# Optimization experiments

Hardware: AMD Instinct MI355X
Metric: run time of the kernel (lower is better)

The kernel has to match this reference:

```python
import jax, jax.numpy as jnp
import numpy as np

DIM = 512
HEADS = 8
HEAD_DIM = DIM // HEADS
SR = 2
LN_EPS = 1e-3  # keras LayerNormalization default epsilon


def setup_inputs() -> dict:
    key = jax.random.key(0)
    ks = jax.random.split(key, 12)
    B, N = 4, 64 * 64
    s = lambda fan_in: 1.0 / np.sqrt(fan_in)
    return {
        "x": jax.random.normal(ks[0], (B, N, DIM), dtype=jnp.float32),
        "H": 64,
        "W": 64,
        "Wq": jax.random.normal(ks[1], (DIM, DIM), jnp.float32) * s(DIM),
        "bq": jnp.zeros((DIM,), jnp.float32),
        "Wkv": jax.random.normal(ks[2], (DIM, 2 * DIM), jnp.float32) * s(DIM),
        "bkv": jnp.zeros((2 * DIM,), jnp.float32),
        "Wp": jax.random.normal(ks[3], (DIM, DIM), jnp.float32) * s(DIM),
        "bp": jnp.zeros((DIM,), jnp.float32),
        "sr_kernel": jax.random.normal(ks[4], (SR, SR, DIM, DIM), jnp.float32) * s(SR * SR * DIM),
        "sr_bias": jnp.zeros((DIM,), jnp.float32),
        "gamma": jnp.ones((DIM,), jnp.float32),
        "beta": jnp.zeros((DIM,), jnp.float32),
    }


def _layer_norm(x, gamma, beta):
    mu = jnp.mean(x, axis=-1, keepdims=True)
    var = jnp.mean(jnp.square(x - mu), axis=-1, keepdims=True)
    return (x - mu) * jax.lax.rsqrt(var + LN_EPS) * gamma + beta


def reference(x, H, W, Wq, bq, Wkv, bkv, Wp, bp, sr_kernel, sr_bias, gamma, beta):
    B, N, C = x.shape
    scale = HEAD_DIM ** -0.5

    # q projection -> [B, heads, N, head_dim]
    q = (x @ Wq + bq).reshape(B, N, HEADS, HEAD_DIM).transpose(0, 2, 1, 3)

    # sequence reduction: strided conv (kernel=stride=SR, SAME padding) + LayerNorm
    x_ = x.reshape(B, H, W, C)
    x_ = jax.lax.conv_general_dilated(
        x_, sr_kernel, window_strides=(SR, SR), padding="SAME",
        dimension_numbers=("NHWC", "HWIO", "NHWC")) + sr_bias
    x_ = x_.reshape(B, -1, C)           # [B, N_kv, C]
    x_ = _layer_norm(x_, gamma, beta)

    # kv projection -> k, v: [B, heads, N_kv, head_dim]
    kv = (x_ @ Wkv + bkv).reshape(B, -1, 2, HEADS, HEAD_DIM).transpose(2, 0, 3, 1, 4)
    k, v = kv[0], kv[1]

    attn = jnp.einsum("bhnd,bhmd->bhnm", q, k) * scale
    attn = jax.nn.softmax(attn, axis=-1)
    out = jnp.einsum("bhnm,bhmd->bhnd", attn, v)  # [B, heads, N, head_dim]
    out = out.transpose(0, 2, 1, 3).reshape(B, N, C)
    return out @ Wp + bp
```

## Files before the change

### kernel.cpp

```cpp
#include <hip/hip_runtime.h>
#include <math.h>

#define BDIM   4
#define NTOK   4096
#define CDIM   512
#define NHEADS 8
#define HDIM   64
#define NKV    1024
#define HPIX   64
#define WPIX   64

typedef __attribute__((ext_vector_type(8)))  short    short8;
typedef __attribute__((ext_vector_type(4)))  float    floatx4;
typedef __attribute__((ext_vector_type(16))) float    floatx16;
typedef __attribute__((ext_vector_type(4)))  unsigned uintx4;
typedef unsigned short ushort_t;

static __device__ inline unsigned short f2bf(float f) {
  unsigned u = __float_as_uint(f);
  unsigned r = (u + 0x7fffu + ((u >> 16) & 1u)) >> 16;
  return (unsigned short)r;
}

static __device__ inline unsigned cvt_pk_bf16(float lo, float hi) {
  unsigned r;
  asm volatile("v_cvt_pk_bf16_f32 %0, %1, %2" : "=v"(r) : "v"(lo), "v"(hi));
  return r;
}

static __device__ inline void pl32_swap(unsigned& a, unsigned& b) {
  asm volatile("v_permlane32_swap_b32 %0, %1" : "+v"(a), "+v"(b));
}

static __device__ inline void gload16(const void* g, void* l) {
  __builtin_amdgcn_global_load_lds(
      (const __attribute__((address_space(1))) void*)g,
      (__attribute__((address_space(3))) void*)l, 16, 0, 0);
}

__global__ __launch_bounds__(256) void prep_kernel(
    const float* __restrict__ x, ushort_t* __restrict__ xb,
    const float* __restrict__ Wq, const float* __restrict__ Wkv,
    const float* __restrict__ Wp, const float* __restrict__ srk,
    ushort_t* __restrict__ Wqt, ushort_t* __restrict__ Wkvt,
    ushort_t* __restrict__ Wpt, ushort_t* __restrict__ srkt) {
  const int bid = blockIdx.x;
  if (bid < 4096) {
    const size_t i = ((size_t)bid * 256 + threadIdx.x) * 8;
    float4 f0 = *(const float4*)&x[i];
    float4 f1 = *(const float4*)&x[i + 4];
    short8 v;
    v[0] = (short)f2bf(f0.x); v[1] = (short)f2bf(f0.y);
    v[2] = (short)f2bf(f0.z); v[3] = (short)f2bf(f0.w);
    v[4] = (short)f2bf(f1.x); v[5] = (short)f2bf(f1.y);
    v[6] = (short)f2bf(f1.z); v[7] = (short)f2bf(f1.w);
    *(short8*)&xb[i] = v;
    return;
  }
  __shared__ float t[32][33];
  const int tb = bid - 4096;
  const float* in; ushort_t* outp; int C, tile;
  if (tb < 256)       { in = Wq;  outp = Wqt;  C = 512;  tile = tb; }
  else if (tb < 768)  { in = Wkv; outp = Wkvt; C = 1024; tile = tb - 256; }
  else if (tb < 1024) { in = Wp;  outp = Wpt;  C = 512;  tile = tb - 768; }
  else                { in = srk; outp = srkt; C = 512;  tile = tb - 1024; }
  const int R = (tb >= 1024) ? 2048 : 512;
  const int tcn = C >> 5;
  const int r0 = (tile / tcn) * 32, c0 = (tile % tcn) * 32;
  const int tr = threadIdx.x & 31, tc = threadIdx.x >> 5;
#pragma unroll
  for (int i = 0; i < 4; ++i)
    t[tc + 8 * i][tr] = in[(size_t)(r0 + tc + 8 * i) * C + c0 + tr];
  __syncthreads();
#pragma unroll
  for (int i = 0; i < 4; ++i)
    outp[(size_t)(c0 + tc + 8 * i) * R + r0 + tr] = f2bf(t[tr][tc + 8 * i]);
}

__global__ __launch_bounds__(256) void gemm_bf16(
    const ushort_t* __restrict__ A, const ushort_t* __restrict__ Bt,
    const float* __restrict__ bias, float* __restrict__ Cf,
    ushort_t* __restrict__ Cb, int M, int N, int K, float scale) {
  __shared__ char As[16384];
  __shared__ char Bs[16384];
  const int tid = threadIdx.x;
  const int w = tid >> 6, lane = tid & 63;
  const int g = lane >> 4, qr = lane & 15;
  const int wr = w >> 1, wc = w & 1;
  const int row0 = blockIdx.x * 128, col0 = blockIdx.y * 128;
  const int rl = w * 8 + (lane >> 3);
  const int sch = (lane & 7) ^ ((lane >> 3) & 7);

  floatx4 acc[4][4] = {};

  for (int k0 = 0; k0 < K; k0 += 64) {
    __syncthreads();
#pragma unroll
    for (int i = 0; i < 4; ++i) {
      const int r = rl + 32 * i;
      const unsigned lb = (unsigned)(w * 1024 + i * 4096);
      gload16(&A[(size_t)(row0 + r) * K + k0 + sch * 8], As + lb);
      gload16(&Bt[(size_t)(col0 + r) * K + k0 + sch * 8], Bs + lb);
    }
    __syncthreads();

#pragma unroll
    for (int kc = 0; kc < 2; ++kc) {
      short8 af[4], bfr[4];
#pragma unroll
      for (int mi = 0; mi < 4; ++mi) {
        const int r = wr * 64 + mi * 16 + qr;
        af[mi] = *(const short8*)(As +
            ((unsigned)(r * 128 + kc * 64 + g * 16) ^ (unsigned)((r & 7) << 4)));
      }
#pragma unroll
      for (int ni = 0; ni < 4; ++ni) {
        const int c = wc * 64 + ni * 16 + qr;
        bfr[ni] = *(const short8*)(Bs +
            ((unsigned)(c * 128 + kc * 64 + g * 16) ^ (unsigned)((c & 7) << 4)));
      }
#pragma unroll
      for (int mi = 0; mi < 4; ++mi)
#pragma unroll
        for (int ni = 0; ni < 4; ++ni)
          acc[mi][ni] = __builtin_amdgcn_mfma_f32_16x16x32_bf16(
              af[mi], bfr[ni], acc[mi][ni], 0, 0, 0);
    }
  }

#pragma unroll
  for (int mi = 0; mi < 4; ++mi) {
#pragma unroll
    for (int ni = 0; ni < 4; ++ni) {
      const int col = col0 + wc * 64 + ni * 16 + qr;
      const float bv = bias[col];
#pragma unroll
      for (int ri = 0; ri < 4; ++ri) {
        const int row = row0 + wr * 64 + mi * 16 + g * 4 + ri;
        const float v = (acc[mi][ni][ri] + bv) * scale;
        if (Cb) Cb[(size_t)row * N + col] = f2bf(v);
        else    Cf[(size_t)row * N + col] = v;
      }
    }
  }
}

__global__ __launch_bounds__(256) void gemm_kv(
    const ushort_t* __restrict__ A, const ushort_t* __restrict__ Bt,
    const float* __restrict__ bias, char* __restrict__ Kimg,
    char* __restrict__ Vimg) {
  __shared__ char As[16384];
  __shared__ char Bs[16384];
  const int tid = threadIdx.x;
  const int w = tid >> 6, lane = tid & 63;
  const int g = lane >> 4, qr = lane & 15;
  const int wr = w >> 1, wc = w & 1;
  const int row0 = blockIdx.x * 128, col0 = blockIdx.y * 128;
  const int rl = w * 8 + (lane >> 3);
  const int sch = (lane & 7) ^ ((lane >> 3) & 7);

  floatx4 acc[4][4] = {};

  for (int k0 = 0; k0 < 512; k0 += 64) {
    __syncthreads();
#pragma unroll
    for (int i = 0; i < 4; ++i) {
      const int r = rl + 32 * i;
      const unsigned lb = (unsigned)(w * 1024 + i * 4096);
      gload16(&A[(size_t)(row0 + r) * 512 + k0 + sch * 8], As + lb);
      gload16(&Bt[(size_t)(col0 + r) * 512 + k0 + sch * 8], Bs + lb);
    }
    __syncthreads();

#pragma unroll
    for (int kc = 0; kc < 2; ++kc) {
      short8 af[4], bfr[4];
#pragma unroll
      for (int mi = 0; mi < 4; ++mi) {
        const int r = wr * 64 + mi * 16 + qr;
        af[mi] = *(const short8*)(As +
            ((unsigned)(r * 128 + kc * 64 + g * 16) ^ (unsigned)((r & 7) << 4)));
      }
#pragma unroll
      for (int ni = 0; ni < 4; ++ni) {
        const int c = wc * 64 + ni * 16 + qr;
        bfr[ni] = *(const short8*)(Bs +
            ((unsigned)(c * 128 + kc * 64 + g * 16) ^ (unsigned)((c & 7) << 4)));
      }
#pragma unroll
      for (int mi = 0; mi < 4; ++mi)
#pragma unroll
        for (int ni = 0; ni < 4; ++ni)
          acc[mi][ni] = __builtin_amdgcn_mfma_f32_16x16x32_bf16(
              af[mi], bfr[ni], acc[mi][ni], 0, 0, 0);
    }
  }

#pragma unroll
  for (int mi = 0; mi < 4; ++mi) {
#pragma unroll
    for (int ni = 0; ni < 4; ++ni) {
      const int col = col0 + wc * 64 + ni * 16 + qr;
      const float bv = bias[col];
#pragma unroll
      for (int ri = 0; ri < 4; ++ri) {
        const int row = row0 + wr * 64 + mi * 16 + g * 4 + ri;
        const ushort_t v = f2bf(acc[mi][ni][ri] + bv);
        const int b = row >> 10, m = row & 1023;
        const int t = m >> 6, mr = m & 63;
        const int st = mr >> 5;
        if (col < 512) {
          const int h = col >> 6, d = col & 63;
          const int ql = mr & 31;
          const int ks = d >> 4, hi2 = (d >> 3) & 1, j = d & 7;
          char* img = Kimg + (((size_t)(b * NHEADS + h) * 16 + t) << 13);
          *(ushort_t*)(img + (unsigned)(((st * 4 + ks) << 10) +
                       ((hi2 << 5) + ql) * 16 + j * 2)) = v;
        } else {
          const int c = col - 512, h = c >> 6, d = c & 63;
          const int r5 = mr & 31;
          const int hf16 = r5 >> 4, rem = r5 & 15;
          const int hi2 = rem >> 3, cc = (rem >> 1) & 3, odd = rem & 1;
          const int db = d >> 5, ql = d & 31;
          char* img = Vimg + (((size_t)(b * NHEADS + h) * 16 + t) << 13);
          *(ushort_t*)(img + (unsigned)(((st * 4 + db * 2 + hf16) << 10) +
                       ((hi2 << 5) + ql) * 16 + cc * 4 + odd * 2)) = v;
        }
      }
    }
  }
}

__global__ __launch_bounds__(256) void conv_gemm(
    const ushort_t* __restrict__ xb, const ushort_t* __restrict__ Bt,
    const float* __restrict__ bias, float* __restrict__ Cf) {
  __shared__ char As[16384];
  __shared__ char Bs[8192];
  const int tid = threadIdx.x;
  const int w = tid >> 6, lane = tid & 63;
  const int g = lane >> 4, qr = lane & 15;
  const int wr = w >> 1, wc = w & 1;
  const int row0 = blockIdx.x * 128, col0 = blockIdx.y * 64;
  const int rl = w * 8 + (lane >> 3);
  const int sch = (lane & 7) ^ ((lane >> 3) & 7);

  floatx4 acc[4][2] = {};

  for (int k0 = 0; k0 < 2048; k0 += 64) {
    __syncthreads();
    {
      const int di = k0 >> 10, dj = (k0 >> 9) & 1, cib = (k0 & 511) + sch * 8;
#pragma unroll
      for (int i = 0; i < 4; ++i) {
        const int r = rl + 32 * i;
        const int gr = row0 + r;
        const int bb = gr >> 10, p = gr & 1023;
        const int oi = p >> 5, oj = p & 31;
        const size_t off =
            ((size_t)((bb * HPIX + 2 * oi + di) * WPIX + 2 * oj + dj)) * CDIM + cib;
        gload16(&xb[off], As + (unsigned)(w * 1024 + i * 4096));
      }
#pragma unroll
      for (int i = 0; i < 2; ++i) {
        const int r = rl + 32 * i;
        gload16(&Bt[(size_t)(col0 + r) * 2048 + k0 + sch * 8],
                Bs + (unsigned)(w * 1024 + i * 4096));
      }
    }
    __syncthreads();

#pragma unroll
    for (int kc = 0; kc < 2; ++kc) {
      short8 af[4], bfr[2];
#pragma unroll
      for (int mi = 0; mi < 4; ++mi) {
        const int r = wr * 64 + mi * 16 + qr;
        af[mi] = *(const short8*)(As +
            ((unsigned)(r * 128 + kc * 64 + g * 16) ^ (unsigned)((r & 7) << 4)));
      }
#pragma unroll
      for (int ni = 0; ni < 2; ++ni) {
        const int c = wc * 32 + ni * 16 + qr;
        bfr[ni] = *(const short8*)(Bs +
            ((unsigned)(c * 128 + kc * 64 + g * 16) ^ (unsigned)((c & 7) << 4)));
      }
#pragma unroll
      for (int mi = 0; mi < 4; ++mi)
#pragma unroll
        for (int ni = 0; ni < 2; ++ni)
          acc[mi][ni] = __builtin_amdgcn_mfma_f32_16x16x32_bf16(
              af[mi], bfr[ni], acc[mi][ni], 0, 0, 0);
    }
  }

#pragma unroll
  for (int mi = 0; mi < 4; ++mi) {
#pragma unroll
    for (int ni = 0; ni < 2; ++ni) {
      const int col = col0 + wc * 32 + ni * 16 + qr;
      const float bv = bias[col];
#pragma unroll
      for (int ri = 0; ri < 4; ++ri) {
        const int row = row0 + wr * 64 + mi * 16 + g * 4 + ri;
        Cf[(size_t)row * 512 + col] = acc[mi][ni][ri] + bv;
      }
    }
  }
}

__global__ __launch_bounds__(256) void ln_kernel(
    const float* __restrict__ in, ushort_t* __restrict__ out,
    const float* __restrict__ gamma, const float* __restrict__ beta) {
  const int row = blockIdx.x * 4 + (threadIdx.x >> 6);
  const int lane = threadIdx.x & 63;
  const float* p = in + (size_t)row * CDIM;
  float v[8];
  float s = 0.f;
#pragma unroll
  for (int j = 0; j < 8; ++j) { v[j] = p[lane + j * 64]; s += v[j]; }
#pragma unroll
  for (int o = 32; o > 0; o >>= 1) s += __shfl_xor(s, o);
  const float mu = s * (1.0f / 512.0f);
  float vs = 0.f;
#pragma unroll
  for (int j = 0; j < 8; ++j) { const float d = v[j] - mu; vs += d * d; }
#pragma unroll
  for (int o = 32; o > 0; o >>= 1) vs += __shfl_xor(vs, o);
  const float rstd = rsqrtf(vs * (1.0f / 512.0f) + 1e-3f);
  ushort_t* q = out + (size_t)row * CDIM;
#pragma unroll
  for (int j = 0; j < 8; ++j) {
    const int c = lane + j * 64;
    q[c] = f2bf((v[j] - mu) * rstd * gamma[c] + beta[c]);
  }
}

__global__ __launch_bounds__(256) void attn_kernel(
    const ushort_t* __restrict__ Q, const char* __restrict__ Kimg,
    const char* __restrict__ Vimg, ushort_t* __restrict__ AO) {
  __shared__ char Ks[16384];
  __shared__ char Vt[16384];
  __shared__ float red[4][32];

  const int b = blockIdx.z, h = blockIdx.y;
  const int q0 = blockIdx.x * 128;
  const int tid = threadIdx.x;
  const int w = tid >> 6, lane = tid & 63;
  const int ql = lane & 31;
  const int hi = lane >> 5;
  const unsigned lbyte = (unsigned)(lane * 16);

  short8 qf[4];
  {
    const ushort_t* qp = &Q[((size_t)(b * NTOK + q0 + 32 * w + ql)) * CDIM + h * HDIM];
#pragma unroll
    for (int ks = 0; ks < 4; ++ks)
      qf[ks] = *(const short8*)&qp[ks * 16 + hi * 8];
  }

  const char* kbase = Kimg + (((size_t)(b * NHEADS + h)) << 17);
  const char* vbase = Vimg + (((size_t)(b * NHEADS + h)) << 17);

  floatx16 Oacc[2] = {};
  float l0 = 0.f, l1 = 0.f;

  for (int t2 = 0; t2 < NKV / 128; ++t2) {
    __syncthreads();
    {
      const char* kg = kbase + ((size_t)t2 << 14) + w * 4096 + lane * 16;
      const char* vg = vbase + ((size_t)t2 << 14) + w * 4096 + lane * 16;
      char* kd = Ks + w * 4096;
      char* vd = Vt + w * 4096;
#pragma unroll
      for (int i = 0; i < 4; ++i) {
        gload16(kg + i * 1024, kd + i * 1024);
        gload16(vg + i * 1024, vd + i * 1024);
      }
    }
    __syncthreads();

#pragma unroll
    for (int sub = 0; sub < 2; ++sub) {
      const char* ksb = Ks + sub * 8192 + lbyte;
      const char* vtb = Vt + sub * 8192 + lbyte;

      floatx16 sacc[2];
      __builtin_amdgcn_s_setprio(1);
#pragma unroll
      for (int st = 0; st < 2; ++st) {
        floatx16 s_ = {};
#pragma unroll
        for (int ks = 0; ks < 4; ++ks) {
          short8 kf = *(const short8*)(ksb + ((st * 4 + ks) << 10));
          s_ = __builtin_amdgcn_mfma_f32_32x32x16_bf16(kf, qf[ks], s_, 0, 0, 0);
        }
        sacc[st] = s_;
      }
      __builtin_amdgcn_s_setprio(0);

#pragma unroll
      for (int st = 0; st < 2; ++st) {
        unsigned W[8];
#pragma unroll
        for (int i = 0; i < 8; ++i) {
          const float pa = __builtin_amdgcn_exp2f(sacc[st][2 * i]);
          const float pb = __builtin_amdgcn_exp2f(sacc[st][2 * i + 1]);
          l0 += pa; l1 += pb;
          W[i] = cvt_pk_bf16(pa, pb);
        }
        pl32_swap(W[0], W[2]); pl32_swap(W[1], W[3]);
        pl32_swap(W[4], W[6]); pl32_swap(W[5], W[7]);
        uintx4 u0 = {W[0], W[1], W[2], W[3]};
        uintx4 u1 = {W[4], W[5], W[6], W[7]};
        const short8 pa0 = __builtin_bit_cast(short8, u0);
        const short8 pa1 = __builtin_bit_cast(short8, u1);
        __builtin_amdgcn_s_setprio(1);
#pragma unroll
        for (int db = 0; db < 2; ++db) {
          short8 v0 = *(const short8*)(vtb + ((st * 4 + db * 2) << 10));
          short8 v1 = *(const short8*)(vtb + ((st * 4 + db * 2 + 1) << 10));
          Oacc[db] = __builtin_amdgcn_mfma_f32_32x32x16_bf16(pa0, v0, Oacc[db], 0, 0, 0);
          Oacc[db] = __builtin_amdgcn_mfma_f32_32x32x16_bf16(pa1, v1, Oacc[db], 0, 0, 0);
        }
        __builtin_amdgcn_s_setprio(0);
      }
    }
  }

  float lrun = l0 + l1;
  lrun += __shfl_xor(lrun, 32);
  if (hi == 0) red[w][ql] = 1.0f / lrun;
  asm volatile("s_waitcnt lgkmcnt(0)" ::: "memory");
  __builtin_amdgcn_sched_barrier(0);
#pragma unroll
  for (int r = 0; r < 16; ++r) {
    const int qrow = (r & 3) + 8 * (r >> 2) + 4 * hi;
    const float iv = red[w][qrow];
    const size_t rowoff =
        ((size_t)(b * NTOK + q0 + 32 * w + qrow)) * CDIM + h * HDIM;
    AO[rowoff + ql]      = f2bf(Oacc[0][r] * iv);
    AO[rowoff + 32 + ql] = f2bf(Oacc[1][r] * iv);
  }
}

extern "C" void kernel_launch(void* const* d_in, const int* in_sizes, int n_in,
                              void* d_out, int out_size, void* d_ws, size_t ws_size,
                              hipStream_t stream) {
  const float* x     = (const float*)d_in[0];
  const float* Wq    = (const float*)d_in[3];
  const float* bq    = (const float*)d_in[4];
  const float* Wkv   = (const float*)d_in[5];
  const float* bkv   = (const float*)d_in[6];
  const float* Wp    = (const float*)d_in[7];
  const float* bp    = (const float*)d_in[8];
  const float* srk   = (const float*)d_in[9];
  const float* srb   = (const float*)d_in[10];
  const float* gamma = (const float*)d_in[11];
  const float* beta  = (const float*)d_in[12];
  float* out = (float*)d_out;

  ushort_t* xb   = (ushort_t*)d_ws;
  ushort_t* Qb   = xb + (size_t)16384 * 512;
  ushort_t* AOb  = Qb + (size_t)16384 * 512;
  float*    XR   = (float*)(AOb + (size_t)16384 * 512);
  ushort_t* XL   = (ushort_t*)(XR + (size_t)4096 * 512);
  char*     Kimg = (char*)(XL + (size_t)4096 * 512);
  char*     Vimg = Kimg + (size_t)4 * 8 * 16 * 8192;
  ushort_t* Wqt  = (ushort_t*)(Vimg + (size_t)4 * 8 * 16 * 8192);
  ushort_t* Wkvt = Wqt + (size_t)512 * 512;
  ushort_t* Wpt  = Wkvt + (size_t)1024 * 512;
  ushort_t* srkt = Wpt + (size_t)512 * 512;

  prep_kernel<<<4096 + 2048, 256, 0, stream>>>(
      x, xb, Wq, Wkv, Wp, srk, Wqt, Wkvt, Wpt, srkt);

  gemm_bf16<<<dim3(16384 / 128, 512 / 128), 256, 0, stream>>>(
      xb, Wqt, bq, nullptr, Qb, 16384, 512, 512, 0.125f * 1.44269504f);
  conv_gemm<<<dim3(4096 / 128, 512 / 64), 256, 0, stream>>>(xb, srkt, srb, XR);
  ln_kernel<<<4096 / 4, 256, 0, stream>>>(XR, XL, gamma, beta);
  gemm_kv<<<dim3(4096 / 128, 1024 / 128), 256, 0, stream>>>(
      XL, Wkvt, bkv, Kimg, Vimg);
  attn_kernel<<<dim3(NTOK / 128, NHEADS, BDIM), 256, 0, stream>>>(Qb, Kimg, Vimg, AOb);
  gemm_bf16<<<dim3(16384 / 128, 512 / 128), 256, 0, stream>>>(
      AOb, Wpt, bp, out, nullptr, 16384, 512, 512, 1.0f);
}
```

Measured before the change: 139.3 us.

## Merge Q projection and SR conv GEMM into one launch; MFMA row-sum in attention

Merges the Q-projection GEMM and the strided-conv GEMM into a single launch. Conv blocks come first, so the long K=2048 conv tiles start early and the shorter Q tiles fill the remaining CUs, removing one launch and the tail gap between the two kernels. In attention, the softmax denominator is now built by an extra MFMA that multiplies P by a vector of ones. This replaces the per-lane scalar adds, the cross-lane shuffle and the LDS reduction. It adds two extra MFMAs per tile, and the row sums now come from bf16-rounded probabilities.

```diff
diff --git a/kernel.cpp b/kernel.cpp
--- a/kernel.cpp
+++ b/kernel.cpp
@@ -140,6 +140,141 @@
         const float v = (acc[mi][ni][ri] + bv) * scale;
         if (Cb) Cb[(size_t)row * N + col] = f2bf(v);
         else    Cf[(size_t)row * N + col] = v;
+      }
+    }
+  }
+}
+
+__global__ __launch_bounds__(256) void qconv_gemm(
+    const ushort_t* __restrict__ xb, const ushort_t* __restrict__ srkt,
+    const float* __restrict__ srb, float* __restrict__ XR,
+    const ushort_t* __restrict__ Wqt, const float* __restrict__ bq,
+    ushort_t* __restrict__ Qb, float qscale) {
+  __shared__ char As[16384];
+  __shared__ char Bs[16384];
+  const int tid = threadIdx.x;
+  const int w = tid >> 6, lane = tid & 63;
+  const int g = lane >> 4, qr = lane & 15;
+  const int wr = w >> 1, wc = w & 1;
+  const int rl = w * 8 + (lane >> 3);
+  const int sch = (lane & 7) ^ ((lane >> 3) & 7);
+
+  if (blockIdx.x < 256) {
+    const int cb = blockIdx.x;
+    const int row0 = (cb & 31) * 128, col0 = (cb >> 5) * 64;
+    floatx4 acc[4][2] = {};
+
+    for (int k0 = 0; k0 < 2048; k0 += 64) {
+      __syncthreads();
+      {
+        const int di = k0 >> 10, dj = (k0 >> 9) & 1, cib = (k0 & 511) + sch * 8;
+#pragma unroll
+        for (int i = 0; i < 4; ++i) {
+          const int r = rl + 32 * i;
+          const int gr = row0 + r;
+          const int bb = gr >> 10, p = gr & 1023;
+          const int oi = p >> 5, oj = p & 31;
+          const size_t off =
+              ((size_t)((bb * HPIX + 2 * oi + di) * WPIX + 2 * oj + dj)) * CDIM + cib;
+          gload16(&xb[off], As + (unsigned)(w * 1024 + i * 4096));
+        }
+#pragma unroll
+        for (int i = 0; i < 2; ++i) {
+          const int r = rl + 32 * i;
+          gload16(&srkt[(size_t)(col0 + r) * 2048 + k0 + sch * 8],
+                  Bs + (unsigned)(w * 1024 + i * 4096));
+        }
+      }
+      __syncthreads();
+
+#pragma unroll
+      for (int kc = 0; kc < 2; ++kc) {
+        short8 af[4], bfr[2];
+#pragma unroll
+        for (int mi = 0; mi < 4; ++mi) {
+          const int r = wr * 64 + mi * 16 + qr;
+          af[mi] = *(const short8*)(As +
+              ((unsigned)(r * 128 + kc * 64 + g * 16) ^ (unsigned)((r & 7) << 4)));
+        }
+#pragma unroll
+        for (int ni = 0; ni < 2; ++ni) {
+          const int c = wc * 32 + ni * 16 + qr;
+          bfr[ni] = *(const short8*)(Bs +
+              ((unsigned)(c * 128 + kc * 64 + g * 16) ^ (unsigned)((c & 7) << 4)));
+        }
+#pragma unroll
+        for (int mi = 0; mi < 4; ++mi)
+#pragma unroll
+          for (int ni = 0; ni < 2; ++ni)
+            acc[mi][ni] = __builtin_amdgcn_mfma_f32_16x16x32_bf16(
+                af[mi], bfr[ni], acc[mi][ni], 0, 0, 0);
+      }
+    }
+
+#pragma unroll
+    for (int mi = 0; mi < 4; ++mi) {
+#pragma unroll
+      for (int ni = 0; ni < 2; ++ni) {
+        const int col = col0 + wc * 32 + ni * 16 + qr;
+        const float bv = srb[col];
+#pragma unroll
+        for (int ri = 0; ri < 4; ++ri) {
+          const int row = row0 + wr * 64 + mi * 16 + g * 4 + ri;
+          XR[(size_t)row * 512 + col] = acc[mi][ni][ri] + bv;
+        }
+      }
+    }
+  } else {
+    const int qb = blockIdx.x - 256;
+    const int row0 = (qb & 127) * 128, col0 = (qb >> 7) * 128;
+    floatx4 acc[4][4] = {};
+
+    for (int k0 = 0; k0 < 512; k0 += 64) {
+      __syncthreads();
+#pragma unroll
+      for (int i = 0; i < 4; ++i) {
+        const int r = rl + 32 * i;
+        const unsigned lb = (unsigned)(w * 1024 + i * 4096);
+        gload16(&xb[(size_t)(row0 + r) * 512 + k0 + sch * 8], As + lb);
+        gload16(&Wqt[(size_t)(col0 + r) * 512 + k0 + sch * 8], Bs + lb);
+      }
+      __syncthreads();
+
+#pragma unroll
+      for (int kc = 0; kc < 2; ++kc) {
+        short8 af[4], bfr[4];
+#pragma unroll
+        for (int mi = 0; mi < 4; ++mi) {
+          const int r = wr * 64 + mi * 16 + qr;
+          af[mi] = *(const short8*)(As +
+              ((unsigned)(r * 128 + kc * 64 + g * 16) ^ (unsigned)((r & 7) << 4)));
+        }
+#pragma unroll
+        for (int ni = 0; ni < 4; ++ni) {
+          const int c = wc * 64 + ni * 16 + qr;
+          bfr[ni] = *(const short8*)(Bs +
+              ((unsigned)(c * 128 + kc * 64 + g * 16) ^ (unsigned)((c & 7) << 4)));
+        }
+#pragma unroll
+        for (int mi = 0; mi < 4; ++mi)
+#pragma unroll
+          for (int ni = 0; ni < 4; ++ni)
+            acc[mi][ni] = __builtin_amdgcn_mfma_f32_16x16x32_bf16(
+                af[mi], bfr[ni], acc[mi][ni], 0, 0, 0);
+      }
+    }
+
+#pragma unroll
+    for (int mi = 0; mi < 4; ++mi) {
+#pragma unroll
+      for (int ni = 0; ni < 4; ++ni) {
+        const int col = col0 + wc * 64 + ni * 16 + qr;
+        const float bv = bq[col];
+#pragma unroll
+        for (int ri = 0; ri < 4; ++ri) {
+          const int row = row0 + wr * 64 + mi * 16 + g * 4 + ri;
+          Qb[(size_t)row * 512 + col] = f2bf((acc[mi][ni][ri] + bv) * qscale);
+        }
       }
     }
   }
@@ -231,83 +366,6 @@
   }
 }
 
-__global__ __launch_bounds__(256) void conv_gemm(
-    const ushort_t* __restrict__ xb, const ushort_t* __restrict__ Bt,
-    const float* __restrict__ bias, float* __restrict__ Cf) {
-  __shared__ char As[16384];
-  __shared__ char Bs[8192];
-  const int tid = threadIdx.x;
-  const int w = tid >> 6, lane = tid & 63;
-  const int g = lane >> 4, qr = lane & 15;
-  const int wr = w >> 1, wc = w & 1;
-  const int row0 = blockIdx.x * 128, col0 = blockIdx.y * 64;
-  const int rl = w * 8 + (lane >> 3);
-  const int sch = (lane & 7) ^ ((lane >> 3) & 7);
-
-  floatx4 acc[4][2] = {};
-
-  for (int k0 = 0; k0 < 2048; k0 += 64) {
-    __syncthreads();
-    {
-      const int di = k0 >> 10, dj = (k0 >> 9) & 1, cib = (k0 & 511) + sch * 8;
-#pragma unroll
-      for (int i = 0; i < 4; ++i) {
-        const int r = rl + 32 * i;
-        const int gr = row0 + r;
-        const int bb = gr >> 10, p = gr & 1023;
-        const int oi = p >> 5, oj = p & 31;
-        const size_t off =
-            ((size_t)((bb * HPIX + 2 * oi + di) * WPIX + 2 * oj + dj)) * CDIM + cib;
-        gload16(&xb[off], As + (unsigned)(w * 1024 + i * 4096));
-      }
-#pragma unroll
-      for (int i = 0; i < 2; ++i) {
-        const int r = rl + 32 * i;
-        gload16(&Bt[(size_t)(col0 + r) * 2048 + k0 + sch * 8],
-                Bs + (unsigned)(w * 1024 + i * 4096));
-      }
-    }
-    __syncthreads();
-
-#pragma unroll
-    for (int kc = 0; kc < 2; ++kc) {
-      short8 af[4], bfr[2];
-#pragma unroll
-      for (int mi = 0; mi < 4; ++mi) {
-        const int r = wr * 64 + mi * 16 + qr;
-        af[mi] = *(const short8*)(As +
-            ((unsigned)(r * 128 + kc * 64 + g * 16) ^ (unsigned)((r & 7) << 4)));
-      }
-#pragma unroll
-      for (int ni = 0; ni < 2; ++ni) {
-        const int c = wc * 32 + ni * 16 + qr;
-        bfr[ni] = *(const short8*)(Bs +
-            ((unsigned)(c * 128 + kc * 64 + g * 16) ^ (unsigned)((c & 7) << 4)));
-      }
-#pragma unroll
-      for (int mi = 0; mi < 4; ++mi)
-#pragma unroll
-        for (int ni = 0; ni < 2; ++ni)
-          acc[mi][ni] = __builtin_amdgcn_mfma_f32_16x16x32_bf16(
-              af[mi], bfr[ni], acc[mi][ni], 0, 0, 0);
-    }
-  }
-
-#pragma unroll
-  for (int mi = 0; mi < 4; ++mi) {
-#pragma unroll
-    for (int ni = 0; ni < 2; ++ni) {
-      const int col = col0 + wc * 32 + ni * 16 + qr;
-      const float bv = bias[col];
-#pragma unroll
-      for (int ri = 0; ri < 4; ++ri) {
-        const int row = row0 + wr * 64 + mi * 16 + g * 4 + ri;
-        Cf[(size_t)row * 512 + col] = acc[mi][ni][ri] + bv;
-      }
-    }
-  }
-}
-
 __global__ __launch_bounds__(256) void ln_kernel(
     const float* __restrict__ in, ushort_t* __restrict__ out,
     const float* __restrict__ gamma, const float* __restrict__ beta) {
@@ -340,7 +398,6 @@
     const char* __restrict__ Vimg, ushort_t* __restrict__ AO) {
   __shared__ char Ks[16384];
   __shared__ char Vt[16384];
-  __shared__ float red[4][32];
 
   const int b = blockIdx.z, h = blockIdx.y;
   const int q0 = blockIdx.x * 128;
@@ -358,11 +415,15 @@
       qf[ks] = *(const short8*)&qp[ks * 16 + hi * 8];
   }
 
+  short8 ones;
+#pragma unroll
+  for (int i = 0; i < 8; ++i) ones[i] = (short)0x3F80;
+
   const char* kbase = Kimg + (((size_t)(b * NHEADS + h)) << 17);
   const char* vbase = Vimg + (((size_t)(b * NHEADS + h)) << 17);
 
   floatx16 Oacc[2] = {};
-  float l0 = 0.f, l1 = 0.f;
+  floatx16 Lacc = {};
 
   for (int t2 = 0; t2 < NKV / 128; ++t2) {
     __syncthreads();
@@ -405,7 +466,6 @@
         for (int i = 0; i < 8; ++i) {
           const float pa = __builtin_amdgcn_exp2f(sacc[st][2 * i]);
           const float pb = __builtin_amdgcn_exp2f(sacc[st][2 * i + 1]);
-          l0 += pa; l1 += pb;
           W[i] = cvt_pk_bf16(pa, pb);
         }
         pl32_swap(W[0], W[2]); pl32_swap(W[1], W[3]);
@@ -422,20 +482,17 @@
           Oacc[db] = __builtin_amdgcn_mfma_f32_32x32x16_bf16(pa0, v0, Oacc[db], 0, 0, 0);
           Oacc[db] = __builtin_amdgcn_mfma_f32_32x32x16_bf16(pa1, v1, Oacc[db], 0, 0, 0);
         }
+        Lacc = __builtin_amdgcn_mfma_f32_32x32x16_bf16(pa0, ones, Lacc, 0, 0, 0);
+        Lacc = __builtin_amdgcn_mfma_f32_32x32x16_bf16(pa1, ones, Lacc, 0, 0, 0);
         __builtin_amdgcn_s_setprio(0);
       }
     }
   }
 
-  float lrun = l0 + l1;
-  lrun += __shfl_xor(lrun, 32);
-  if (hi == 0) red[w][ql] = 1.0f / lrun;
-  asm volatile("s_waitcnt lgkmcnt(0)" ::: "memory");
-  __builtin_amdgcn_sched_barrier(0);
 #pragma unroll
   for (int r = 0; r < 16; ++r) {
     const int qrow = (r & 3) + 8 * (r >> 2) + 4 * hi;
-    const float iv = red[w][qrow];
+    const float iv = 1.0f / Lacc[r];
     const size_t rowoff =
         ((size_t)(b * NTOK + q0 + 32 * w + qrow)) * CDIM + h * HDIM;
     AO[rowoff + ql]      = f2bf(Oacc[0][r] * iv);
@@ -474,9 +531,8 @@
   prep_kernel<<<4096 + 2048, 256, 0, stream>>>(
       x, xb, Wq, Wkv, Wp, srk, Wqt, Wkvt, Wpt, srkt);
 
-  gemm_bf16<<<dim3(16384 / 128, 512 / 128), 256, 0, stream>>>(
-      xb, Wqt, bq, nullptr, Qb, 16384, 512, 512, 0.125f * 1.44269504f);
-  conv_gemm<<<dim3(4096 / 128, 512 / 64), 256, 0, stream>>>(xb, srkt, srb, XR);
+  qconv_gemm<<<768, 256, 0, stream>>>(
+      xb, srkt, srb, XR, Wqt, bq, Qb, 0.125f * 1.44269504f);
   ln_kernel<<<4096 / 4, 256, 0, stream>>>(XR, XL, gamma, beta);
   gemm_kv<<<dim3(4096 / 128, 1024 / 128), 256, 0, stream>>>(
       XL, Wkvt, bkv, Kimg, Vimg);
```

Result: faster. 126.6 us (-9.1%).
